# Optimization experiments

Hardware: AMD Instinct MI355X
Metric: run time of the kernel (lower is better)

The kernel has to match this reference:

```python
import jax, jax.numpy as jnp
import numpy as np

N, E, G = 50000, 320000, 256
BN_EPS = 1e-5
HEADS = 4


def _bn(x, g, b):
    # eval-mode BatchNorm1d with running_mean=0, running_var=1
    return g * (x * np.float32(1.0 / np.sqrt(1.0 + BN_EPS))) + b


def _mlp(x, w1, b1, w2, b2):
    return jax.nn.relu(x @ w1 + b1) @ w2 + b2


def _gatv2(x, src, dst, ea, lw, lb, rw, rb, ew, att, bias):
    n = x.shape[0]
    H = HEADS
    C = lw.shape[1] // H
    # self-loops with edge_attr = mean of incoming edge features (fill_value='mean')
    deg = jax.ops.segment_sum(jnp.ones((ea.shape[0],), x.dtype), dst, num_segments=n)
    loop_ea = jax.ops.segment_sum(ea, dst, num_segments=n) / jnp.maximum(deg, 1.0)[:, None]
    ar = jnp.arange(n)
    s = jnp.concatenate([src, ar])
    d = jnp.concatenate([dst, ar])
    ea_all = jnp.concatenate([ea, loop_ea], axis=0)
    xl = (x @ lw + lb).reshape(n, H, C)   # lin_l (source / message features)
    xr = (x @ rw + rb).reshape(n, H, C)   # lin_r (target)
    ee = (ea_all @ ew).reshape(-1, H, C)  # lin_edge (no bias)
    m = jax.nn.leaky_relu(xl[s] + xr[d] + ee, 0.2)       # [E+N, H, C]
    a = jnp.einsum('ehc,hc->eh', m, att)                 # attention logits
    amax = jax.ops.segment_max(a, d, num_segments=n)
    ex = jnp.exp(a - amax[d])
    den = jax.ops.segment_sum(ex, d, num_segments=n)
    w = ex / den[d]                                      # scatter-softmax over target
    out = jax.ops.segment_sum(xl[s] * w[..., None], d, num_segments=n)
    return out.reshape(n, H * C) + bias


def _meta(x, ea, u, src, dst, batch, ep, gp, up):
    # EdgeModel -> NodeModel(GATv2 + relu) -> GlobalModel (residuals=False, eval dropout)
    ea2 = _mlp(jnp.concatenate([x[src], x[dst], ea], axis=1), *ep)
    xn = jax.nn.relu(_gatv2(x, src, dst, ea2, *gp))
    pooled = jax.ops.segment_sum(xn, batch, num_segments=G)
    u2 = _mlp(jnp.concatenate([u, pooled], axis=1), *up)
    return xn, ea2, u2


def _forward(x, edge_attr, e1_w1, e1_b1, e1_w2, e1_b2, g1_lw, g1_lb, g1_rw, g1_rb, g1_ew, g1_att, g1_bias, u1_w1, u1_b1, u1_w2, u1_b2, bn_n_g, bn_n_b, bn_e_g, bn_e_b, bn_u_g, bn_u_b, e2_w1, e2_b1, e2_w2, e2_b2, g2_lw, g2_lb, g2_rw, g2_rb, g2_ew, g2_att, g2_bias, u2_w1, u2_b1, u2_w2, u2_b2, fc1_w, fc1_b, fc2_w, fc2_b, src, dst, batch):
    u0 = jnp.zeros((G, 256), x.dtype)
    x1, ea1, u1 = _meta(x, edge_attr, u0, src, dst, batch,
                        (e1_w1, e1_b1, e1_w2, e1_b2),
                        (g1_lw, g1_lb, g1_rw, g1_rb, g1_ew, g1_att, g1_bias),
                        (u1_w1, u1_b1, u1_w2, u1_b2))
    x1 = _bn(x1, bn_n_g, bn_n_b)
    ea1 = _bn(ea1, bn_e_g, bn_e_b)
    u1 = _bn(u1, bn_u_g, bn_u_b)
    _, _, u2 = _meta(x1, ea1, u1, src, dst, batch,
                     (e2_w1, e2_b1, e2_w2, e2_b2),
                     (g2_lw, g2_lb, g2_rw, g2_rb, g2_ew, g2_att, g2_bias),
                     (u2_w1, u2_b1, u2_w2, u2_b2))
    h = jax.nn.relu(u2 @ fc1_w + fc1_b)
    return h @ fc2_w + fc2_b


def setup_inputs() -> dict:
    key = jax.random.key(0)
    ks = iter(jax.random.split(key, 64))
    rp = lambda shape: jax.random.normal(next(ks), shape, jnp.float32) * 0.05
    inp = {}
    inp['x'] = jax.random.normal(next(ks), (N, 64), jnp.float32)
    inp['edge_attr'] = jax.random.normal(next(ks), (E, 16), jnp.float32)
    # layer 1: EdgeModel(64,16,h=64,out=128), GATv2(64->256,H=4,edge=128), Global(256+256->256)
    inp.update(e1_w1=rp((144, 64)), e1_b1=rp((64,)), e1_w2=rp((64, 128)), e1_b2=rp((128,)))
    inp.update(g1_lw=rp((64, 256)), g1_lb=rp((256,)), g1_rw=rp((64, 256)), g1_rb=rp((256,)),
               g1_ew=rp((128, 256)), g1_att=rp((4, 64)), g1_bias=rp((256,)))
    inp.update(u1_w1=rp((512, 256)), u1_b1=rp((256,)), u1_w2=rp((256, 256)), u1_b2=rp((256,)))
    inp.update(bn_n_g=jnp.ones((256,), jnp.float32), bn_n_b=jnp.zeros((256,), jnp.float32),
               bn_e_g=jnp.ones((128,), jnp.float32), bn_e_b=jnp.zeros((128,), jnp.float32),
               bn_u_g=jnp.ones((256,), jnp.float32), bn_u_b=jnp.zeros((256,), jnp.float32))
    # layer 2: EdgeModel(256,128,h=128,out=128), GATv2(256->256,H=4,edge=128), Global
    inp.update(e2_w1=rp((640, 128)), e2_b1=rp((128,)), e2_w2=rp((128, 128)), e2_b2=rp((128,)))
    inp.update(g2_lw=rp((256, 256)), g2_lb=rp((256,)), g2_rw=rp((256, 256)), g2_rb=rp((256,)),
               g2_ew=rp((128, 256)), g2_att=rp((4, 64)), g2_bias=rp((256,)))
    inp.update(u2_w1=rp((512, 256)), u2_b1=rp((256,)), u2_w2=rp((256, 256)), u2_b2=rp((256,)))
    inp.update(fc1_w=rp((256, 64)), fc1_b=rp((64,)), fc2_w=rp((64, 1)), fc2_b=rp((1,)))
    inp['edge_index'] = jax.random.randint(next(ks), (2, E), 0, N, jnp.int64)
    inp['batch'] = jnp.sort(jax.random.randint(next(ks), (N,), 0, G, jnp.int64))
    return inp


def reference(x, edge_attr, e1_w1, e1_b1, e1_w2, e1_b2, g1_lw, g1_lb, g1_rw, g1_rb, g1_ew, g1_att, g1_bias, u1_w1, u1_b1, u1_w2, u1_b2, bn_n_g, bn_n_b, bn_e_g, bn_e_b, bn_u_g, bn_u_b, e2_w1, e2_b1, e2_w2, e2_b2, g2_lw, g2_lb, g2_rw, g2_rb, g2_ew, g2_att, g2_bias, u2_w1, u2_b1, u2_w2, u2_b2, fc1_w, fc1_b, fc2_w, fc2_b, edge_index, batch):
    return _forward(x, edge_attr, e1_w1, e1_b1, e1_w2, e1_b2, g1_lw, g1_lb, g1_rw, g1_rb, g1_ew, g1_att, g1_bias, u1_w1, u1_b1, u1_w2, u1_b2, bn_n_g, bn_n_b, bn_e_g, bn_e_b, bn_u_g, bn_u_b, e2_w1, e2_b1, e2_w2, e2_b2, g2_lw, g2_lb, g2_rw, g2_rb, g2_ew, g2_att, g2_bias, u2_w1, u2_b1, u2_w2, u2_b2, fc1_w, fc1_b, fc2_w, fc2_b, edge_index[0], edge_index[1], batch)
```

## Files before the change

kernel.cpp:

```cpp
#include <hip/hip_runtime.h>
#include <hip/hip_bf16.h>
#include <hip/hip_fp8.h>
#include <cstdint>
#include <cstddef>

#define INVS 0.99999500003749968f
#define G_GRAPHS 256

using bf16 = __hip_bfloat16;
using short8 = __attribute__((ext_vector_type(8))) short;
using floatx4 = __attribute__((ext_vector_type(4))) float;

__device__ __forceinline__ unsigned short f2bf(float v) {
    union { float f; unsigned u; } x; x.f = v;
    unsigned r = x.u + 0x7fffu + ((x.u >> 16) & 1u);
    return (unsigned short)(r >> 16);
}
__device__ __forceinline__ float bfu(unsigned short u) { return __uint_as_float((unsigned)u << 16); }
__device__ __forceinline__ unsigned char f2fp8(float v) {
    __hip_fp8_e4m3 q(v); return q.__x;
}
__device__ __forceinline__ float fp82f(unsigned char b) {
    __hip_fp8_e4m3 q; q.__x = b; return (float)q;
}

__global__ void degi_k(const int* __restrict__ dst, int* __restrict__ degi, int E) {
    int gid = blockIdx.x * 256 + threadIdx.x;
    if (gid < E) atomicAdd(&degi[dst[gid]], 1);
}

__global__ __launch_bounds__(1024) void scan_blk_k(const int* __restrict__ degi,
                                                   int* __restrict__ off,
                                                   int* __restrict__ bsum, int N) {
    __shared__ int buf[1024];
    int t = threadIdx.x;
    int base = blockIdx.x * 2048;
    int i0 = base + 2 * t, i1 = base + 2 * t + 1;
    int v0 = (i0 < N) ? (degi[i0] + 1) : 0;
    int v1 = (i1 < N) ? (degi[i1] + 1) : 0;
    int s = v0 + v1;
    buf[t] = s;
    __syncthreads();
    for (int ofs = 1; ofs < 1024; ofs <<= 1) {
        int add = (t >= ofs) ? buf[t - ofs] : 0;
        __syncthreads();
        buf[t] += add;
        __syncthreads();
    }
    int excl = buf[t] - s;
    if (i0 < N) off[i0] = excl;
    if (i1 < N) off[i1] = excl + v0;
    if (t == 1023) bsum[blockIdx.x] = buf[1023];
}

__global__ void scan_top_k(const int* __restrict__ bsum, int* __restrict__ boff,
                           int* __restrict__ off, int NBLK, int N) {
    if (threadIdx.x == 0 && blockIdx.x == 0) {
        int run = 0;
        for (int i = 0; i < NBLK; ++i) { boff[i] = run; run += bsum[i]; }
        off[N] = run;
    }
}

__global__ void scan_add_k(int* __restrict__ off, const int* __restrict__ boff, int N) {
    int gid = blockIdx.x * 256 + threadIdx.x;
    if (gid < N) off[gid] += boff[gid >> 11];
}

__global__ void fill_csr_k(const int* __restrict__ src, const int* __restrict__ dst,
                           const int* __restrict__ off, int* __restrict__ fillc,
                           int* __restrict__ csr_src, int* __restrict__ csr_dst,
                           int* __restrict__ csr_eid, int* __restrict__ slot_of,
                           int E, int N) {
    int gid = blockIdx.x * 256 + threadIdx.x;
    if (gid < E) {
        int d = dst[gid];
        int slot = off[d] + atomicAdd(&fillc[d], 1);
        csr_src[slot] = src[gid];
        csr_dst[slot] = d;
        csr_eid[slot] = gid;
        slot_of[gid] = slot;
    }
    if (gid < N) {
        int slot = off[gid + 1] - 1;
        csr_src[slot] = gid;
        csr_dst[slot] = gid;
        csr_eid[slot] = E + gid;
    }
}

__global__ void conv_weights1_k(const float* __restrict__ w1, const float* __restrict__ w2,
                                short* __restrict__ w1s, short* __restrict__ w2s) {
    int gid = blockIdx.x * 256 + threadIdx.x;
    if (gid < 1280) {
        int f = gid >> 6, lane = gid & 63;
        int kk = f >> 2, tt = f & 3;
        int n = tt * 16 + (lane & 15);
        int k0 = kk * 32 + (lane >> 4) * 8;
        short8 v;
        for (int j = 0; j < 8; ++j) {
            int k = k0 + j;
            v[j] = (k < 144) ? (short)f2bf(w1[k * 64 + n]) : (short)0;
        }
        *(short8*)(w1s + (long long)gid * 8) = v;
    } else if (gid < 2304) {
        int g2 = gid - 1280;
        int f = g2 >> 6, lane = g2 & 63;
        int kk = f >> 3, tt = f & 7;
        int n = tt * 16 + (lane & 15);
        int k0 = kk * 32 + (lane >> 4) * 8;
        short8 v;
        for (int j = 0; j < 8; ++j) v[j] = (short)f2bf(w2[(k0 + j) * 128 + n]);
        *(short8*)(w2s + (long long)g2 * 8) = v;
    }
}

__global__ void conv_ew_k(const float* __restrict__ ew, short* __restrict__ ews) {
    int gid = blockIdx.x * 256 + threadIdx.x;
    if (gid >= 4096) return;
    int f = gid >> 6, lane = gid & 63;
    int kk = f >> 4, tt = f & 15;
    int n = tt * 16 + (lane & 15);
    int k0 = kk * 32 + (lane >> 4) * 8;
    short8 v;
    for (int j = 0; j < 8; ++j) v[j] = (short)f2bf(ew[(k0 + j) * 256 + n]);
    *(short8*)(ews + (long long)gid * 8) = v;
}

template <int K>
__global__ void conv_nodew_k(const float* __restrict__ wl, const float* __restrict__ wr,
                             short* __restrict__ out) {
    int gid = blockIdx.x * 256 + threadIdx.x;
    if (gid >= (K / 32) * 32 * 64) return;
    int f = gid >> 6, lane = gid & 63;
    int kk = f >> 5, tt = f & 31;
    int n = tt * 16 + (lane & 15);
    int k0 = kk * 32 + (lane >> 4) * 8;
    short8 v;
    for (int j = 0; j < 8; ++j) {
        int k = k0 + j;
        float x = (n < 256) ? wl[k * 256 + n] : wr[k * 256 + (n - 256)];
        v[j] = (short)f2bf(x);
    }
    *(short8*)(out + (long long)gid * 8) = v;
}

__global__ void conv_pre2w_k(const float* __restrict__ w1, short* __restrict__ out) {
    int gid = blockIdx.x * 256 + threadIdx.x;
    if (gid >= 8 * 16 * 64) return;
    int f = gid >> 6, lane = gid & 63;
    int kk = f >> 4, tt = f & 15;
    int n = tt * 16 + (lane & 15);
    int k0 = kk * 32 + (lane >> 4) * 8;
    short8 v;
    for (int j = 0; j < 8; ++j) {
        int k = k0 + j;
        float x = (n < 128) ? w1[k * 128 + n] : w1[(256 + k) * 128 + (n - 128)];
        v[j] = (short)f2bf(x);
    }
    *(short8*)(out + (long long)gid * 8) = v;
}

__global__ __launch_bounds__(256) void edge_mlp1_mfma_k(
    const float* __restrict__ x, const float* __restrict__ ea,
    const int* __restrict__ src, const int* __restrict__ dst,
    const int* __restrict__ slot_of,
    const short* __restrict__ w1s, const float* __restrict__ b1,
    const short* __restrict__ w2s, const float* __restrict__ b2,
    const short* __restrict__ ews,
    bf16* __restrict__ out, unsigned char* __restrict__ ee8, int E) {
    __shared__ short At[32][168];
    __shared__ short Ht[32][72];
    __shared__ unsigned char Et[32][272];
    __shared__ int sdv[32][2];
    __shared__ int slt[32];
    int t = threadIdx.x;
    long long e0 = (long long)blockIdx.x * 32;
    if (t < 64) {
        int r = t & 31;
        long long e = e0 + r;
        int v = 0;
        if (e < E) v = (t < 32) ? src[e] : dst[e];
        sdv[r][t >> 5] = v;
    } else if (t < 96) {
        int r = t - 64;
        long long e = e0 + r;
        slt[r] = (e < E) ? slot_of[e] : -1;
    }
    __syncthreads();
    for (int i = t; i < 32 * 40; i += 256) {
        int r = i / 40, c = i - r * 40;
        long long e = e0 + r;
        float4 v = {0.f, 0.f, 0.f, 0.f};
        if (e < E) {
            if (c < 16)      v = *(const float4*)(x + (long long)sdv[r][0] * 64 + c * 4);
            else if (c < 32) v = *(const float4*)(x + (long long)sdv[r][1] * 64 + (c - 16) * 4);
            else if (c < 36) v = *(const float4*)(ea + e * 16 + (c - 32) * 4);
        }
        ushort4 pk;
        pk.x = f2bf(v.x); pk.y = f2bf(v.y); pk.z = f2bf(v.z); pk.w = f2bf(v.w);
        *(ushort4*)&At[r][c * 4] = pk;
    }
    __syncthreads();

    int w = t >> 6, lane = t & 63;
    int m0 = (w & 1) * 16;
    int lr = lane & 15, lq = lane >> 4;

    int nq1 = (w >> 1) * 2;
    floatx4 acc[2];
    for (int i = 0; i < 2; ++i) acc[i] = (floatx4){0.f, 0.f, 0.f, 0.f};
    for (int kk = 0; kk < 5; ++kk) {
        short8 a = *(const short8*)&At[m0 + lr][kk * 32 + lq * 8];
        for (int tt = 0; tt < 2; ++tt) {
            short8 b = *(const short8*)(w1s + ((long long)((kk * 4 + nq1 + tt) * 64 + lane)) * 8);
            acc[tt] = __builtin_amdgcn_mfma_f32_16x16x32_bf16(a, b, acc[tt], 0, 0, 0);
        }
    }
    for (int tt = 0; tt < 2; ++tt) {
        int col = (nq1 + tt) * 16 + lr;
        float bv = b1[col];
        for (int r = 0; r < 4; ++r)
            Ht[m0 + lq * 4 + r][col] = (short)f2bf(fmaxf(acc[tt][r] + bv, 0.f));
    }
    __syncthreads();

    int nq2 = (w >> 1) * 4;
    floatx4 acc2[4];
    for (int i = 0; i < 4; ++i) acc2[i] = (floatx4){0.f, 0.f, 0.f, 0.f};
    for (int kk = 0; kk < 2; ++kk) {
        short8 a = *(const short8*)&Ht[m0 + lr][kk * 32 + lq * 8];
        for (int tt = 0; tt < 4; ++tt) {
            short8 b = *(const short8*)(w2s + ((long long)((kk * 8 + nq2 + tt) * 64 + lane)) * 8);
            acc2[tt] = __builtin_amdgcn_mfma_f32_16x16x32_bf16(a, b, acc2[tt], 0, 0, 0);
        }
    }
    for (int tt = 0; tt < 4; ++tt) {
        int col = (nq2 + tt) * 16 + lr;
        float bv = b2[col];
        for (int r = 0; r < 4; ++r)
            At[m0 + lq * 4 + r][col] = (short)f2bf(acc2[tt][r] + bv);
    }
    __syncthreads();
    {
        int nq3 = (w >> 1) * 8;
        floatx4 acc3[8];
        for (int i = 0; i < 8; ++i) acc3[i] = (floatx4){0.f, 0.f, 0.f, 0.f};
        for (int kk = 0; kk < 4; ++kk) {
            short8 a = *(const short8*)&At[m0 + lr][kk * 32 + lq * 8];
            for (int tt = 0; tt < 8; ++tt) {
                short8 b = *(const short8*)(ews + ((long long)((kk * 16 + nq3 + tt) * 64 + lane)) * 8);
                acc3[tt] = __builtin_amdgcn_mfma_f32_16x16x32_bf16(a, b, acc3[tt], 0, 0, 0);
            }
        }
        for (int tt = 0; tt < 8; ++tt) {
            int col = (nq3 + tt) * 16 + lr;
            for (int r = 0; r < 4; ++r)
                Et[m0 + lq * 4 + r][col] = f2fp8(acc3[tt][r]);
        }
    }
    for (int i = t; i < 512; i += 256) {
        int r = i >> 4, c = i & 15;
        int s = slt[r];
        if (s >= 0)
            *(short8*)(void*)(out + (long long)s * 128 + c * 8) = *(const short8*)&At[r][c * 8];
    }
    __syncthreads();
    for (int i = t; i < 512; i += 256) {
        int r = i >> 4, c = i & 15;
        int s = slt[r];
        if (s >= 0)
            *(uint4*)(ee8 + (long long)s * 256 + c * 16) = *(const uint4*)&Et[r][c * 16];
    }
}

template <int K, typename T>
__global__ __launch_bounds__(256) void node_linear_mfma_k(
    const T* x, const short* __restrict__ ws,
    const float* __restrict__ bl, const float* __restrict__ br,
    bf16* __restrict__ xl, bf16* xr, int N) {
    __shared__ short At[16][K + 8];
    __shared__ short Ot[16][520];
    int t = threadIdx.x;
    long long n0 = (long long)blockIdx.x * 16;
    if (sizeof(T) == 4) {
        for (int i = t; i < 16 * (K / 4); i += 256) {
            int r = i / (K / 4), c = i % (K / 4);
            long long n = n0 + r;
            float4 v = {0.f, 0.f, 0.f, 0.f};
            if (n < N) v = *(const float4*)((const float*)x + n * K + c * 4);
            ushort4 pk;
            pk.x = f2bf(v.x); pk.y = f2bf(v.y); pk.z = f2bf(v.z); pk.w = f2bf(v.w);
            *(ushort4*)&At[r][c * 4] = pk;
        }
    } else {
        for (int i = t; i < 16 * (K / 8); i += 256) {
            int r = i / (K / 8), c = i % (K / 8);
            long long n = n0 + r;
            short8 v = {0, 0, 0, 0, 0, 0, 0, 0};
            if (n < N) v = *(const short8*)(const void*)((const bf16*)x + n * K + c * 8);
            *(short8*)&At[r][c * 8] = v;
        }
    }
    __syncthreads();

    int w = t >> 6, lane = t & 63;
    int nq = w * 8;
    int lr = lane & 15, lq = lane >> 4;

    floatx4 acc[8];
    for (int i = 0; i < 8; ++i) acc[i] = (floatx4){0.f, 0.f, 0.f, 0.f};
    for (int kk = 0; kk < K / 32; ++kk) {
        short8 a = *(const short8*)&At[lr][kk * 32 + lq * 8];
        for (int tt = 0; tt < 8; ++tt) {
            short8 b = *(const short8*)(ws + ((long long)((kk * 32 + nq + tt) * 64 + lane)) * 8);
            acc[tt] = __builtin_amdgcn_mfma_f32_16x16x32_bf16(a, b, acc[tt], 0, 0, 0);
        }
    }
    for (int tt = 0; tt < 8; ++tt) {
        int col = (nq + tt) * 16 + lr;
        float bv = (col < 256) ? bl[col] : br[col - 256];
        for (int r = 0; r < 4; ++r)
            Ot[lq * 4 + r][col] = (short)f2bf(acc[tt][r] + bv);
    }
    __syncthreads();
    for (int i = t; i < 1024; i += 256) {
        int r = i >> 6, c = i & 63;
        long long n = n0 + r;
        if (n < N) {
            short8 v = *(const short8*)&Ot[r][c * 8];
            if (c < 32) *(short8*)(void*)(xl + n * 256 + c * 8) = v;
            else        *(short8*)(void*)(xr + n * 256 + (c - 32) * 8) = v;
        }
    }
}

__global__ __launch_bounds__(256) void pre_mfma_k(
    const bf16* __restrict__ x, const short* __restrict__ ws,
    const float* __restrict__ bx, bf16* __restrict__ out, int N) {
    __shared__ short At[16][264];
    __shared__ short Ot[16][264];
    int t = threadIdx.x;
    long long n0 = (long long)blockIdx.x * 16;
    for (int i = t; i < 512; i += 256) {
        int r = i >> 5, c = i & 31;
        long long n = n0 + r;
        short8 v = {0, 0, 0, 0, 0, 0, 0, 0};
        if (n < N) v = *(const short8*)(const void*)(x + n * 256 + c * 8);
        *(short8*)&At[r][c * 8] = v;
    }
    __syncthreads();

    int w = t >> 6, lane = t & 63;
    int nq = w * 4;
    int lr = lane & 15, lq = lane >> 4;

    floatx4 acc[4];
    for (int i = 0; i < 4; ++i) acc[i] = (floatx4){0.f, 0.f, 0.f, 0.f};
    for (int kk = 0; kk < 8; ++kk) {
        short8 a = *(const short8*)&At[lr][kk * 32 + lq * 8];
        for (int tt = 0; tt < 4; ++tt) {
            short8 b = *(const short8*)(ws + ((long long)((kk * 16 + nq + tt) * 64 + lane)) * 8);
            acc[tt] = __builtin_amdgcn_mfma_f32_16x16x32_bf16(a, b, acc[tt], 0, 0, 0);
        }
    }
    for (int tt = 0; tt < 4; ++tt) {
        int col = (nq + tt) * 16 + lr;
        float bv = bx[col];
        for (int r = 0; r < 4; ++r)
            Ot[lq * 4 + r][col] = (short)f2bf(acc[tt][r] + bv);
    }
    __syncthreads();
    for (int i = t; i < 512; i += 256) {
        int r = i >> 5, c = i & 31;
        long long n = n0 + r;
        if (n < N)
            *(short8*)(void*)(out + n * 256 + c * 8) = *(const short8*)&Ot[r][c * 8];
    }
}

template <bool L1>
__global__ __launch_bounds__(256) void gat_fused_k(
    const unsigned char* __restrict__ ee8, const bf16* __restrict__ xl, const bf16* xr,
    const int* __restrict__ off, const int* __restrict__ csr_src,
    const float* __restrict__ att, const float* __restrict__ bias,
    const float* __restrict__ bng, const float* __restrict__ bnb,
    const int* __restrict__ batch,
    bf16* x1bn, float* __restrict__ pooled, int N) {
    __shared__ float ps[4][260];
    __shared__ int bid[4];
    int t = threadIdx.x;
    int w = t >> 6, lane = t & 63;
    int n = blockIdx.x * 4 + w;
    bool valid = n < N;
    int c0 = lane * 4;
    float o0 = 0.f, o1 = 0.f, o2 = 0.f, o3 = 0.f;
    if (valid) {
        ushort4 xrp = *(const ushort4*)(const void*)(xr + (long long)n * 256 + c0);
        ushort4 xop = *(const ushort4*)(const void*)(xl + (long long)n * 256 + c0);
        float xr0 = bfu(xrp.x), xr1 = bfu(xrp.y), xr2 = bfu(xrp.z), xr3 = bfu(xrp.w);
        float4 atv = *(const float4*)(att + c0);
        float a0 = 0.f, a1 = 0.f, a2 = 0.f, a3 = 0.f, dacc = 0.f;
        float es0 = 0.f, es1 = 0.f, es2 = 0.f, es3 = 0.f;
        int beg = off[n], end1 = off[n + 1] - 1;
        ushort4 xlp;
        unsigned ep;
        {
            int sid = csr_src[beg];
            xlp = *(const ushort4*)(const void*)(xl + (long long)sid * 256 + c0);
            ep = *(const unsigned*)(ee8 + (long long)beg * 256 + c0);
        }
        for (int i = beg; i < end1; ++i) {
            ushort4 cx = xlp;
            unsigned ce = ep;
            if (i + 1 < end1) {
                int sid = csr_src[i + 1];
                xlp = *(const ushort4*)(const void*)(xl + (long long)sid * 256 + c0);
                ep = *(const unsigned*)(ee8 + (long long)(i + 1) * 256 + c0);
            }
            float x0 = bfu(cx.x), x1 = bfu(cx.y), x2 = bfu(cx.z), x3 = bfu(cx.w);
            float e0 = fp82f(ce & 0xff);
            float e1 = fp82f((ce >> 8) & 0xff);
            float e2 = fp82f((ce >> 16) & 0xff);
            float e3 = fp82f(ce >> 24);
            es0 += e0; es1 += e1; es2 += e2; es3 += e3;
            float m0 = x0 + xr0 + e0;
            float m1 = x1 + xr1 + e1;
            float m2 = x2 + xr2 + e2;
            float m3 = x3 + xr3 + e3;
            m0 = m0 > 0.f ? m0 : 0.2f * m0;
            m1 = m1 > 0.f ? m1 : 0.2f * m1;
            m2 = m2 > 0.f ? m2 : 0.2f * m2;
            m3 = m3 > 0.f ? m3 : 0.2f * m3;
            float p = atv.x * m0 + atv.y * m1 + atv.z * m2 + atv.w * m3;
            p += __shfl_xor(p, 1, 64);
            p += __shfl_xor(p, 2, 64);
            p += __shfl_xor(p, 4, 64);
            p += __shfl_xor(p, 8, 64);
            float ex = expf(p);
            a0 += ex * x0; a1 += ex * x1; a2 += ex * x2; a3 += ex * x3;
            dacc += ex;
        }
        {
            float rdv = 1.f / fmaxf((float)(end1 - beg), 1.f);
            float x0 = bfu(xop.x), x1 = bfu(xop.y), x2 = bfu(xop.z), x3 = bfu(xop.w);
            float m0 = x0 + xr0 + es0 * rdv;
            float m1 = x1 + xr1 + es1 * rdv;
            float m2 = x2 + xr2 + es2 * rdv;
            float m3 = x3 + xr3 + es3 * rdv;
            m0 = m0 > 0.f ? m0 : 0.2f * m0;
            m1 = m1 > 0.f ? m1 : 0.2f * m1;
            m2 = m2 > 0.f ? m2 : 0.2f * m2;
            m3 = m3 > 0.f ? m3 : 0.2f * m3;
            float p = atv.x * m0 + atv.y * m1 + atv.z * m2 + atv.w * m3;
            p += __shfl_xor(p, 1, 64);
            p += __shfl_xor(p, 2, 64);
            p += __shfl_xor(p, 4, 64);
            p += __shfl_xor(p, 8, 64);
            float ex = expf(p);
            a0 += ex * x0; a1 += ex * x1; a2 += ex * x2; a3 += ex * x3;
            dacc += ex;
        }
        float inv = 1.f / dacc;
        o0 = fmaxf(a0 * inv + bias[c0],     0.f);
        o1 = fmaxf(a1 * inv + bias[c0 + 1], 0.f);
        o2 = fmaxf(a2 * inv + bias[c0 + 2], 0.f);
        o3 = fmaxf(a3 * inv + bias[c0 + 3], 0.f);
        if (L1) {
            ushort4 o;
            o.x = f2bf(bng[c0]     * (o0 * INVS) + bnb[c0]);
            o.y = f2bf(bng[c0 + 1] * (o1 * INVS) + bnb[c0 + 1]);
            o.z = f2bf(bng[c0 + 2] * (o2 * INVS) + bnb[c0 + 2]);
            o.w = f2bf(bng[c0 + 3] * (o3 * INVS) + bnb[c0 + 3]);
            *(ushort4*)(void*)(x1bn + (long long)n * 256 + c0) = o;
        }
    }
    if (lane == 0) bid[w] = valid ? batch[n] : -1;
    ps[w][c0]     = o0;
    ps[w][c0 + 1] = o1;
    ps[w][c0 + 2] = o2;
    ps[w][c0 + 3] = o3;
    __syncthreads();
    int b0 = bid[0];
    bool same = (b0 >= 0)
             && (bid[1] < 0 || bid[1] == b0)
             && (bid[2] < 0 || bid[2] == b0)
             && (bid[3] < 0 || bid[3] == b0);
    if (same) {
        float s = ps[0][t] + ps[1][t] + ps[2][t] + ps[3][t];
        atomicAdd(&pooled[(long long)b0 * 256 + t], s);
    } else if (valid) {
        long long pb = (long long)bid[w] * 256 + c0;
        atomicAdd(&pooled[pb],     o0);
        atomicAdd(&pooled[pb + 1], o1);
        atomicAdd(&pooled[pb + 2], o2);
        atomicAdd(&pooled[pb + 3], o3);
    }
}

__global__ void global_mlp1_k(const float* __restrict__ pooled,
                              const float* __restrict__ w1, const float* __restrict__ b1,
                              const float* __restrict__ w2, const float* __restrict__ b2,
                              const float* __restrict__ bng, const float* __restrict__ bnb,
                              float* __restrict__ u1bn) {
    __shared__ float pr[256];
    __shared__ float h[256];
    int t = threadIdx.x, g = blockIdx.x;
    pr[t] = pooled[g * 256 + t];
    __syncthreads();
    float acc = b1[t];
    for (int k = 0; k < 256; ++k) acc += pr[k] * w1[(256 + k) * 256 + t];
    h[t] = fmaxf(acc, 0.f);
    __syncthreads();
    float a2 = b2[t];
    for (int k = 0; k < 256; ++k) a2 += h[k] * w2[k * 256 + t];
    u1bn[g * 256 + t] = bng[t] * (a2 * INVS) + bnb[t];
}

__global__ void conv_weights_k(const float* __restrict__ w1, const float* __restrict__ w2,
                               const float* __restrict__ b1,
                               const float* __restrict__ bg, const float* __restrict__ bb,
                               short* __restrict__ w1s, short* __restrict__ w2s,
                               float* __restrict__ b1x) {
    int gid = blockIdx.x * 256 + threadIdx.x;
    if (gid < 10240) {
        int f = gid >> 6, lane = gid & 63;
        int kk = f >> 3, tt = f & 7;
        int n = tt * 16 + (lane & 15);
        int k0 = kk * 32 + (lane >> 4) * 8;
        short8 v;
        for (int j = 0; j < 8; ++j) {
            int k = k0 + j;
            float x = w1[k * 128 + n];
            if (k >= 512) x *= bg[k - 512] * INVS;
            v[j] = (short)f2bf(x);
        }
        *(short8*)(w1s + (long long)gid * 8) = v;
    } else if (gid < 12288) {
        int g2 = gid - 10240;
        int f = g2 >> 6, lane = g2 & 63;
        int kk = f >> 3, tt = f & 7;
        int n = tt * 16 + (lane & 15);
        int k0 = kk * 32 + (lane >> 4) * 8;
        short8 v;
        for (int j = 0; j < 8; ++j) v[j] = (short)f2bf(w2[(k0 + j) * 128 + n]);
        *(short8*)(w2s + (long long)g2 * 8) = v;
    } else if (gid < 12544) {
        int j = gid - 12288;
        b1x[j] = 0.f;
    } else if (gid < 12672) {
        int j = gid - 12544;
        float acc = b1[j];
        for (int c = 0; c < 128; ++c) acc += bb[c] * w1[(512 + c) * 128 + j];
        b1x[128 + j] = acc;
    }
}

__global__ __launch_bounds__(256) void edge_mlp2_mfma_k(
    const bf16* __restrict__ xpre, const bf16* __restrict__ ea_slot,
    const int* __restrict__ csr_src, const int* __restrict__ csr_dst,
    const int* __restrict__ csr_eid,
    const short* __restrict__ w1s,
    const short* __restrict__ w2s, const float* __restrict__ b2,
    const short* __restrict__ ews,
    unsigned char* __restrict__ ee8, int NT, int E) {
    __shared__ float Ps[32][132];
    __shared__ short At[32][136];
    __shared__ short Ht[32][136];
    __shared__ int sdv[32][3];
    unsigned char* Et = (unsigned char*)&Ps[0][0];
    int t = threadIdx.x;
    long long s0 = (long long)blockIdx.x * 32;
    if (t < 96) {
        int r = t & 31, which = t >> 5;
        long long s = s0 + r;
        int v = (which == 2) ? E : 0;
        if (s < NT) v = (which == 0) ? csr_src[s] : (which == 1 ? csr_dst[s] : csr_eid[s]);
        sdv[r][which] = v;
    }
    __syncthreads();
    for (int i = t; i < 512; i += 256) {
        int r = i >> 4, c = i & 15;
        long long s = s0 + r;
        bool ok = (s < NT) && (sdv[r][2] < E);
        float p[8];
        if (ok) {
            short8 vs = *(const short8*)(const void*)(xpre + (long long)sdv[r][0] * 256 + c * 8);
            short8 vd = *(const short8*)(const void*)(xpre + (long long)sdv[r][1] * 256 + 128 + c * 8);
            for (int j = 0; j < 8; ++j)
                p[j] = bfu((unsigned short)vs[j]) + bfu((unsigned short)vd[j]);
        } else {
            for (int j = 0; j < 8; ++j) p[j] = 0.f;
        }
        for (int j = 0; j < 8; ++j) Ps[r][c * 8 + j] = p[j];
    }
    for (int i = t; i < 512; i += 256) {
        int r = i >> 4, c = i & 15;
        long long s = s0 + r;
        short8 v = {0, 0, 0, 0, 0, 0, 0, 0};
        if (s < NT && sdv[r][2] < E)
            v = *(const short8*)(const void*)(ea_slot + s * 128 + c * 8);
        *(short8*)&At[r][c * 8] = v;
    }
    __syncthreads();

    int w = t >> 6, lane = t & 63;
    int m0 = (w & 1) * 16;
    int nq = (w >> 1) * 4;
    int lr = lane & 15, lq = lane >> 4;

    floatx4 acc[4];
    for (int tt = 0; tt < 4; ++tt) {
        int col = (nq + tt) * 16 + lr;
        for (int r = 0; r < 4; ++r) acc[tt][r] = Ps[m0 + lq * 4 + r][col];
    }
    for (int kk = 0; kk < 4; ++kk) {
        short8 a = *(const short8*)&At[m0 + lr][kk * 32 + lq * 8];
        for (int tt = 0; tt < 4; ++tt) {
            short8 b = *(const short8*)(w1s + ((long long)(((16 + kk) * 8 + nq + tt) * 64 + lane)) * 8);
            acc[tt] = __builtin_amdgcn_mfma_f32_16x16x32_bf16(a, b, acc[tt], 0, 0, 0);
        }
    }
    for (int tt = 0; tt < 4; ++tt) {
        int col = (nq + tt) * 16 + lr;
        for (int r = 0; r < 4; ++r)
            Ht[m0 + lq * 4 + r][col] = (short)f2bf(fmaxf(acc[tt][r], 0.f));
    }
    __syncthreads();

    floatx4 acc2[4];
    for (int i = 0; i < 4; ++i) acc2[i] = (floatx4){0.f, 0.f, 0.f, 0.f};
    for (int kk = 0; kk < 4; ++kk) {
        short8 a = *(const short8*)&Ht[m0 + lr][kk * 32 + lq * 8];
        for (int tt = 0; tt < 4; ++tt) {
            short8 b = *(const short8*)(w2s + ((long long)((kk * 8 + nq + tt) * 64 + lane)) * 8);
            acc2[tt] = __builtin_amdgcn_mfma_f32_16x16x32_bf16(a, b, acc2[tt], 0, 0, 0);
        }
    }
    for (int tt = 0; tt < 4; ++tt) {
        int col = (nq + tt) * 16 + lr;
        float bv = b2[col];
        for (int r = 0; r < 4; ++r)
            At[m0 + lq * 4 + r][col] = (short)f2bf(acc2[tt][r] + bv);
    }
    __syncthreads();
    {
        int nq3 = (w >> 1) * 8;
        floatx4 acc3[8];
        for (int i = 0; i < 8; ++i) acc3[i] = (floatx4){0.f, 0.f, 0.f, 0.f};
        for (int kk = 0; kk < 4; ++kk) {
            short8 a = *(const short8*)&At[m0 + lr][kk * 32 + lq * 8];
            for (int tt = 0; tt < 8; ++tt) {
                short8 b = *(const short8*)(ews + ((long long)((kk * 16 + nq3 + tt) * 64 + lane)) * 8);
                acc3[tt] = __builtin_amdgcn_mfma_f32_16x16x32_bf16(a, b, acc3[tt], 0, 0, 0);
            }
        }
        for (int tt = 0; tt < 8; ++tt) {
            int col = (nq3 + tt) * 16 + lr;
            for (int r = 0; r < 4; ++r)
                Et[(m0 + lq * 4 + r) * 272 + col] = f2fp8(acc3[tt][r]);
        }
    }
    __syncthreads();
    for (int i = t; i < 512; i += 256) {
        int r = i >> 4, c = i & 15;
        long long s = s0 + r;
        if (s < NT && sdv[r][2] < E)
            *(uint4*)(ee8 + s * 256 + c * 16) = *(const uint4*)(Et + r * 272 + c * 16);
    }
}

__global__ void final_mlp_k(const float* __restrict__ u1bn, const float* __restrict__ pooled,
                            const float* __restrict__ w1, const float* __restrict__ b1,
                            const float* __restrict__ w2, const float* __restrict__ b2,
                            const float* __restrict__ f1w, const float* __restrict__ f1b,
                            const float* __restrict__ f2w, const float* __restrict__ f2b,
                            float* __restrict__ out) {
    __shared__ float ub[256], pb[256], h[256], u2[256];
    int t = threadIdx.x, g = blockIdx.x;
    ub[t] = u1bn[g * 256 + t];
    pb[t] = pooled[g * 256 + t];
    __syncthreads();
    float acc = b1[t];
    for (int k = 0; k < 256; ++k)
        acc += ub[k] * w1[k * 256 + t] + pb[k] * w1[(256 + k) * 256 + t];
    h[t] = fmaxf(acc, 0.f);
    __syncthreads();
    float a2 = b2[t];
    for (int k = 0; k < 256; ++k) a2 += h[k] * w2[k * 256 + t];
    u2[t] = a2;
    __syncthreads();
    float fv = 0.f;
    if (t < 64) {
        float a3 = f1b[t];
        for (int k = 0; k < 256; ++k) a3 += u2[k] * f1w[k * 64 + t];
        fv = fmaxf(a3, 0.f) * f2w[t];
    }
    for (int off = 32; off; off >>= 1) fv += __shfl_down(fv, off, 64);
    if (t == 0) out[g] = fv + f2b[0];
}

extern "C" void kernel_launch(void* const* d_in, const int* in_sizes, int n_in,
                              void* d_out, int out_size, void* d_ws, size_t ws_size,
                              hipStream_t stream) {
    const float* x         = (const float*)d_in[0];
    const float* edge_attr = (const float*)d_in[1];
    const float* e1_w1 = (const float*)d_in[2];
    const float* e1_b1 = (const float*)d_in[3];
    const float* e1_w2 = (const float*)d_in[4];
    const float* e1_b2 = (const float*)d_in[5];
    const float* g1_lw = (const float*)d_in[6];
    const float* g1_lb = (const float*)d_in[7];
    const float* g1_rw = (const float*)d_in[8];
    const float* g1_rb = (const float*)d_in[9];
    const float* g1_ew = (const float*)d_in[10];
    const float* g1_att = (const float*)d_in[11];
    const float* g1_bias = (const float*)d_in[12];
    const float* u1_w1 = (const float*)d_in[13];
    const float* u1_b1 = (const float*)d_in[14];
    const float* u1_w2 = (const float*)d_in[15];
    const float* u1_b2 = (const float*)d_in[16];
    const float* bn_n_g = (const float*)d_in[17];
    const float* bn_n_b = (const float*)d_in[18];
    const float* bn_e_g = (const float*)d_in[19];
    const float* bn_e_b = (const float*)d_in[20];
    const float* bn_u_g = (const float*)d_in[21];
    const float* bn_u_b = (const float*)d_in[22];
    const float* e2_w1 = (const float*)d_in[23];
    const float* e2_b1 = (const float*)d_in[24];
    const float* e2_w2 = (const float*)d_in[25];
    const float* e2_b2 = (const float*)d_in[26];
    const float* g2_lw = (const float*)d_in[27];
    const float* g2_lb = (const float*)d_in[28];
    const float* g2_rw = (const float*)d_in[29];
    const float* g2_rb = (const float*)d_in[30];
    const float* g2_ew = (const float*)d_in[31];
    const float* g2_att = (const float*)d_in[32];
    const float* g2_bias = (const float*)d_in[33];
    const float* u2_w1 = (const float*)d_in[34];
    const float* u2_b1 = (const float*)d_in[35];
    const float* u2_w2 = (const float*)d_in[36];
    const float* u2_b2 = (const float*)d_in[37];
    const float* fc1_w = (const float*)d_in[38];
    const float* fc1_b = (const float*)d_in[39];
    const float* fc2_w = (const float*)d_in[40];
    const float* fc2_b = (const float*)d_in[41];
    const int* edge_index = (const int*)d_in[42];
    const int* batch = (const int*)d_in[43];

    const int N = in_sizes[0] / 64;
    const int E = in_sizes[1] / 16;
    const int NT = E + N;
    const int G = G_GRAPHS;
    const int* src = edge_index;
    const int* dst = edge_index + E;
    const int NB = (NT + 31) / 32;
    const int NSB = (N + 2047) / 2048;

    char* p = (char*)d_ws;
    auto alloc = [&](size_t bytes) { char* r = p; p += (bytes + 255) & ~(size_t)255; return r; };
    bf16* eabuf = (bf16*)alloc((size_t)NT * 128 * 2);
    bf16* xl    = (bf16*)alloc((size_t)N * 256 * 2);
    bf16* xr    = (bf16*)alloc((size_t)N * 256 * 2);
    bf16* x1bn  = xr;
    unsigned char* ee8 = (unsigned char*)alloc((size_t)NT * 256);
    int* degi   = (int*)alloc((size_t)N * 4);
    int* off    = (int*)alloc((size_t)(N + 1) * 4);
    int* fillc  = (int*)alloc((size_t)N * 4);
    int* csr_src = (int*)alloc((size_t)NT * 4);
    int* csr_dst = (int*)alloc((size_t)NT * 4);
    int* csr_eid = (int*)alloc((size_t)NT * 4);
    int* slot_of = (int*)alloc((size_t)E * 4);
    int* bsum   = (int*)alloc((size_t)(NSB + 1) * 4);
    int* boff   = (int*)alloc((size_t)(NSB + 1) * 4);
    float* pooled = (float*)alloc((size_t)G * 256 * 4);
    float* u1bn = (float*)alloc((size_t)G * 256 * 4);
    short* w1s  = (short*)alloc((size_t)20 * 8 * 64 * 8 * 2);
    short* w2s  = (short*)alloc((size_t)4 * 8 * 64 * 8 * 2);
    float* b1x  = (float*)alloc((size_t)256 * 4);
    short* w1s1 = (short*)alloc((size_t)5 * 4 * 64 * 8 * 2);
    short* w2s1 = (short*)alloc((size_t)2 * 8 * 64 * 8 * 2);
    short* ews1 = (short*)alloc((size_t)4 * 16 * 64 * 8 * 2);
    short* ews2 = (short*)alloc((size_t)4 * 16 * 64 * 8 * 2);
    short* nw1  = (short*)alloc((size_t)2 * 32 * 64 * 8 * 2);
    short* nw2  = (short*)alloc((size_t)8 * 32 * 64 * 8 * 2);
    short* nwp  = (short*)alloc((size_t)8 * 16 * 64 * 8 * 2);

    hipMemsetAsync(degi, 0, (size_t)N * 4, stream);
    hipMemsetAsync(fillc, 0, (size_t)N * 4, stream);
    hipMemsetAsync(pooled, 0, (size_t)G * 256 * 4, stream);
    degi_k<<<(E + 255) / 256, 256, 0, stream>>>(dst, degi, E);
    scan_blk_k<<<NSB, 1024, 0, stream>>>(degi, off, bsum, N);
    scan_top_k<<<1, 64, 0, stream>>>(bsum, boff, off, NSB, N);
    scan_add_k<<<(N + 255) / 256, 256, 0, stream>>>(off, boff, N);
    fill_csr_k<<<(max(E, N) + 255) / 256, 256, 0, stream>>>(src, dst, off, fillc,
                                                            csr_src, csr_dst, csr_eid,
                                                            slot_of, E, N);

    conv_weights1_k<<<9, 256, 0, stream>>>(e1_w1, e1_w2, w1s1, w2s1);
    conv_ew_k<<<16, 256, 0, stream>>>(g1_ew, ews1);
    conv_ew_k<<<16, 256, 0, stream>>>(g2_ew, ews2);
    conv_nodew_k<64><<<16, 256, 0, stream>>>(g1_lw, g1_rw, nw1);
    conv_nodew_k<256><<<64, 256, 0, stream>>>(g2_lw, g2_rw, nw2);
    conv_pre2w_k<<<32, 256, 0, stream>>>(e2_w1, nwp);
    edge_mlp1_mfma_k<<<(E + 31) / 32, 256, 0, stream>>>(x, edge_attr, src, dst, slot_of,
                                                        w1s1, e1_b1, w2s1, e1_b2, ews1,
                                                        eabuf, ee8, E);
    node_linear_mfma_k<64, float><<<(N + 15) / 16, 256, 0, stream>>>(x, nw1, g1_lb, g1_rb, xl, xr, N);
    gat_fused_k<true><<<(N + 3) / 4, 256, 0, stream>>>(ee8, xl, xr, off, csr_src,
                                                       g1_att, g1_bias, bn_n_g, bn_n_b,
                                                       batch, x1bn, pooled, N);
    global_mlp1_k<<<G, 256, 0, stream>>>(pooled, u1_w1, u1_b1, u1_w2, u1_b2, bn_u_g, bn_u_b, u1bn);

    conv_weights_k<<<50, 256, 0, stream>>>(e2_w1, e2_w2, e2_b1, bn_e_g, bn_e_b, w1s, w2s, b1x);
    pre_mfma_k<<<(N + 15) / 16, 256, 0, stream>>>(x1bn, nwp, b1x, xl, N);
    edge_mlp2_mfma_k<<<NB, 256, 0, stream>>>(xl, eabuf, csr_src, csr_dst, csr_eid,
                                             w1s, w2s, e2_b2, ews2, ee8, NT, E);
    node_linear_mfma_k<256, bf16><<<(N + 15) / 16, 256, 0, stream>>>(x1bn, nw2, g2_lb, g2_rb, xl, xr, N);
    hipMemsetAsync(pooled, 0, (size_t)G * 256 * 4, stream);
    gat_fused_k<false><<<(N + 3) / 4, 256, 0, stream>>>(ee8, xl, xr, off, csr_src,
                                                        g2_att, g2_bias, nullptr, nullptr,
                                                        batch, nullptr, pooled, N);
    final_mlp_k<<<G, 256, 0, stream>>>(u1bn, pooled, u2_w1, u2_b1, u2_w2, u2_b2,
                                       fc1_w, fc1_b, fc2_w, fc2_b, (float*)d_out);
}
```

Measured before the change: 847.5 us.

## Precompute per-node first-layer edge MLP projections and iterate edges in CSR order

The first edge MLP layer is split algebraically. x[src]@W1a and x[dst]@W1b + b1 are now computed once per node in a new pre1 kernel, so each edge only gathers two bf16 128-wide rows, adds them, and runs a small K=16 MFMA for the edge-attribute part. The edge kernel now walks CSR slots directly rather than scattering through slot_of, so its stores are contiguous. Self-loop slots are processed with zero inputs. This adds an extra kernel and N×128 bf16 buffer and rounds the node projections to bf16 before summing.

```diff
diff --git a/kernel.cpp b/kernel.cpp
--- a/kernel.cpp
+++ b/kernel.cpp
@@ -70,8 +70,7 @@
 __global__ void fill_csr_k(const int* __restrict__ src, const int* __restrict__ dst,
                            const int* __restrict__ off, int* __restrict__ fillc,
                            int* __restrict__ csr_src, int* __restrict__ csr_dst,
-                           int* __restrict__ csr_eid, int* __restrict__ slot_of,
-                           int E, int N) {
+                           int* __restrict__ csr_eid, int E, int N) {
     int gid = blockIdx.x * 256 + threadIdx.x;
     if (gid < E) {
         int d = dst[gid];
@@ -79,7 +78,6 @@
         csr_src[slot] = src[gid];
         csr_dst[slot] = d;
         csr_eid[slot] = gid;
-        slot_of[gid] = slot;
     }
     if (gid < N) {
         int slot = off[gid + 1] - 1;
@@ -90,19 +88,32 @@
 }
 
 __global__ void conv_weights1_k(const float* __restrict__ w1, const float* __restrict__ w2,
-                                short* __restrict__ w1s, short* __restrict__ w2s) {
+                                short* __restrict__ w1p, short* __restrict__ w1c,
+                                short* __restrict__ w2s) {
     int gid = blockIdx.x * 256 + threadIdx.x;
-    if (gid < 1280) {
+    if (gid < 1024) {
         int f = gid >> 6, lane = gid & 63;
-        int kk = f >> 2, tt = f & 3;
+        int kk = f >> 3, tt = f & 7;
         int n = tt * 16 + (lane & 15);
         int k0 = kk * 32 + (lane >> 4) * 8;
         short8 v;
         for (int j = 0; j < 8; ++j) {
             int k = k0 + j;
-            v[j] = (k < 144) ? (short)f2bf(w1[k * 64 + n]) : (short)0;
-        }
-        *(short8*)(w1s + (long long)gid * 8) = v;
+            float x = (n < 64) ? w1[k * 64 + n] : w1[(64 + k) * 64 + (n - 64)];
+            v[j] = (short)f2bf(x);
+        }
+        *(short8*)(w1p + (long long)gid * 8) = v;
+    } else if (gid < 1280) {
+        int g2 = gid - 1024;
+        int tt = g2 >> 6, lane = g2 & 63;
+        int n = tt * 16 + (lane & 15);
+        int k0 = (lane >> 4) * 8;
+        short8 v;
+        for (int j = 0; j < 8; ++j) {
+            int k = k0 + j;
+            v[j] = (k < 16) ? (short)f2bf(w1[(128 + k) * 64 + n]) : (short)0;
+        }
+        *(short8*)(w1c + (long long)g2 * 8) = v;
     } else if (gid < 2304) {
         int g2 = gid - 1280;
         int f = g2 >> 6, lane = g2 & 63;
@@ -161,93 +172,155 @@
     *(short8*)(out + (long long)gid * 8) = v;
 }
 
-__global__ __launch_bounds__(256) void edge_mlp1_mfma_k(
-    const float* __restrict__ x, const float* __restrict__ ea,
-    const int* __restrict__ src, const int* __restrict__ dst,
-    const int* __restrict__ slot_of,
-    const short* __restrict__ w1s, const float* __restrict__ b1,
-    const short* __restrict__ w2s, const float* __restrict__ b2,
-    const short* __restrict__ ews,
-    bf16* __restrict__ out, unsigned char* __restrict__ ee8, int E) {
-    __shared__ short At[32][168];
-    __shared__ short Ht[32][72];
-    __shared__ unsigned char Et[32][272];
-    __shared__ int sdv[32][2];
-    __shared__ int slt[32];
+__global__ __launch_bounds__(256) void pre1_mfma_k(
+    const float* __restrict__ x, const short* __restrict__ w1p,
+    const float* __restrict__ b1, bf16* __restrict__ pre1, int N) {
+    __shared__ short At[16][72];
+    __shared__ short Ot[16][136];
     int t = threadIdx.x;
-    long long e0 = (long long)blockIdx.x * 32;
-    if (t < 64) {
-        int r = t & 31;
-        long long e = e0 + r;
-        int v = 0;
-        if (e < E) v = (t < 32) ? src[e] : dst[e];
-        sdv[r][t >> 5] = v;
-    } else if (t < 96) {
-        int r = t - 64;
-        long long e = e0 + r;
-        slt[r] = (e < E) ? slot_of[e] : -1;
-    }
-    __syncthreads();
-    for (int i = t; i < 32 * 40; i += 256) {
-        int r = i / 40, c = i - r * 40;
-        long long e = e0 + r;
+    long long n0 = (long long)blockIdx.x * 16;
+    {
+        int r = t >> 4, c = t & 15;
+        long long n = n0 + r;
         float4 v = {0.f, 0.f, 0.f, 0.f};
-        if (e < E) {
-            if (c < 16)      v = *(const float4*)(x + (long long)sdv[r][0] * 64 + c * 4);
-            else if (c < 32) v = *(const float4*)(x + (long long)sdv[r][1] * 64 + (c - 16) * 4);
-            else if (c < 36) v = *(const float4*)(ea + e * 16 + (c - 32) * 4);
-        }
+        if (n < N) v = *(const float4*)(x + n * 64 + c * 4);
         ushort4 pk;
         pk.x = f2bf(v.x); pk.y = f2bf(v.y); pk.z = f2bf(v.z); pk.w = f2bf(v.w);
         *(ushort4*)&At[r][c * 4] = pk;
     }
     __syncthreads();
+    int w = t >> 6, lane = t & 63;
+    int nq = w * 2;
+    int lr = lane & 15, lq = lane >> 4;
+    floatx4 acc[2];
+    for (int i = 0; i < 2; ++i) acc[i] = (floatx4){0.f, 0.f, 0.f, 0.f};
+    for (int kk = 0; kk < 2; ++kk) {
+        short8 a = *(const short8*)&At[lr][kk * 32 + lq * 8];
+        for (int tt = 0; tt < 2; ++tt) {
+            short8 b = *(const short8*)(w1p + ((long long)((kk * 8 + nq + tt) * 64 + lane)) * 8);
+            acc[tt] = __builtin_amdgcn_mfma_f32_16x16x32_bf16(a, b, acc[tt], 0, 0, 0);
+        }
+    }
+    for (int tt = 0; tt < 2; ++tt) {
+        int col = (nq + tt) * 16 + lr;
+        float bv = (col >= 64) ? b1[col - 64] : 0.f;
+        for (int r = 0; r < 4; ++r)
+            Ot[lq * 4 + r][col] = (short)f2bf(acc[tt][r] + bv);
+    }
+    __syncthreads();
+    {
+        int r = t >> 4, c = t & 15;
+        long long n = n0 + r;
+        if (n < N)
+            *(short8*)(void*)(pre1 + n * 128 + c * 8) = *(const short8*)&Ot[r][c * 8];
+    }
+}
+
+__global__ __launch_bounds__(256) void edge_mlp1_mfma_k(
+    const bf16* __restrict__ pre1, const float* __restrict__ ea,
+    const int* __restrict__ csr_src, const int* __restrict__ csr_dst,
+    const int* __restrict__ csr_eid,
+    const short* __restrict__ w1c,
+    const short* __restrict__ w2s, const float* __restrict__ b2,
+    const short* __restrict__ ews,
+    bf16* __restrict__ out, unsigned char* __restrict__ ee8, int NT, int E) {
+    __shared__ float Ps[32][68];
+    __shared__ short Ae[32][40];
+    __shared__ short Ht[32][72];
+    __shared__ short A2[32][136];
+    __shared__ int sdv[32][3];
+    unsigned char* Et = (unsigned char*)&Ps[0][0];
+    int t = threadIdx.x;
+    long long s0 = (long long)blockIdx.x * 32;
+    if (t < 96) {
+        int r = t & 31, which = t >> 5;
+        long long s = s0 + r;
+        int v = (which == 2) ? E : 0;
+        if (s < NT) v = (which == 0) ? csr_src[s] : (which == 1 ? csr_dst[s] : csr_eid[s]);
+        sdv[r][which] = v;
+    }
+    __syncthreads();
+    {
+        int r = t >> 3, c = t & 7;
+        long long s = s0 + r;
+        bool ok = (s < NT) && (sdv[r][2] < E);
+        float p[8];
+        if (ok) {
+            short8 vs = *(const short8*)(const void*)(pre1 + (long long)sdv[r][0] * 128 + c * 8);
+            short8 vd = *(const short8*)(const void*)(pre1 + (long long)sdv[r][1] * 128 + 64 + c * 8);
+            for (int j = 0; j < 8; ++j)
+                p[j] = bfu((unsigned short)vs[j]) + bfu((unsigned short)vd[j]);
+        } else {
+            for (int j = 0; j < 8; ++j) p[j] = 0.f;
+        }
+        for (int j = 0; j < 8; ++j) Ps[r][c * 8 + j] = p[j];
+    }
+    if (t < 128) {
+        int r = t >> 2, c = t & 3;
+        long long s = s0 + r;
+        int eid = sdv[r][2];
+        float4 v = {0.f, 0.f, 0.f, 0.f};
+        if (s < NT && eid < E) v = *(const float4*)(ea + (long long)eid * 16 + c * 4);
+        ushort4 pk;
+        pk.x = f2bf(v.x); pk.y = f2bf(v.y); pk.z = f2bf(v.z); pk.w = f2bf(v.w);
+        *(ushort4*)&Ae[r][c * 4] = pk;
+    } else {
+        int i = t - 128;
+        int r = i >> 2, c = i & 3;
+        *(ushort4*)&Ae[r][16 + c * 4] = (ushort4){0, 0, 0, 0};
+    }
+    __syncthreads();
 
     int w = t >> 6, lane = t & 63;
     int m0 = (w & 1) * 16;
     int lr = lane & 15, lq = lane >> 4;
 
-    int nq1 = (w >> 1) * 2;
-    floatx4 acc[2];
-    for (int i = 0; i < 2; ++i) acc[i] = (floatx4){0.f, 0.f, 0.f, 0.f};
-    for (int kk = 0; kk < 5; ++kk) {
-        short8 a = *(const short8*)&At[m0 + lr][kk * 32 + lq * 8];
+    {
+        int nq1 = (w >> 1) * 2;
+        floatx4 acc[2];
         for (int tt = 0; tt < 2; ++tt) {
-            short8 b = *(const short8*)(w1s + ((long long)((kk * 4 + nq1 + tt) * 64 + lane)) * 8);
+            int col = (nq1 + tt) * 16 + lr;
+            for (int r = 0; r < 4; ++r) acc[tt][r] = Ps[m0 + lq * 4 + r][col];
+        }
+        short8 a = *(const short8*)&Ae[m0 + lr][lq * 8];
+        for (int tt = 0; tt < 2; ++tt) {
+            short8 b = *(const short8*)(w1c + ((long long)((nq1 + tt) * 64 + lane)) * 8);
             acc[tt] = __builtin_amdgcn_mfma_f32_16x16x32_bf16(a, b, acc[tt], 0, 0, 0);
         }
-    }
-    for (int tt = 0; tt < 2; ++tt) {
-        int col = (nq1 + tt) * 16 + lr;
-        float bv = b1[col];
-        for (int r = 0; r < 4; ++r)
-            Ht[m0 + lq * 4 + r][col] = (short)f2bf(fmaxf(acc[tt][r] + bv, 0.f));
-    }
-    __syncthreads();
-
-    int nq2 = (w >> 1) * 4;
-    floatx4 acc2[4];
-    for (int i = 0; i < 4; ++i) acc2[i] = (floatx4){0.f, 0.f, 0.f, 0.f};
-    for (int kk = 0; kk < 2; ++kk) {
-        short8 a = *(const short8*)&Ht[m0 + lr][kk * 32 + lq * 8];
+        for (int tt = 0; tt < 2; ++tt) {
+            int col = (nq1 + tt) * 16 + lr;
+            for (int r = 0; r < 4; ++r)
+                Ht[m0 + lq * 4 + r][col] = (short)f2bf(fmaxf(acc[tt][r], 0.f));
+        }
+    }
+    __syncthreads();
+
+    {
+        int nq2 = (w >> 1) * 4;
+        floatx4 acc2[4];
+        for (int i = 0; i < 4; ++i) acc2[i] = (floatx4){0.f, 0.f, 0.f, 0.f};
+        for (int kk = 0; kk < 2; ++kk) {
+            short8 a = *(const short8*)&Ht[m0 + lr][kk * 32 + lq * 8];
+            for (int tt = 0; tt < 4; ++tt) {
+                short8 b = *(const short8*)(w2s + ((long long)((kk * 8 + nq2 + tt) * 64 + lane)) * 8);
+                acc2[tt] = __builtin_amdgcn_mfma_f32_16x16x32_bf16(a, b, acc2[tt], 0, 0, 0);
+            }
+        }
         for (int tt = 0; tt < 4; ++tt) {
-            short8 b = *(const short8*)(w2s + ((long long)((kk * 8 + nq2 + tt) * 64 + lane)) * 8);
-            acc2[tt] = __builtin_amdgcn_mfma_f32_16x16x32_bf16(a, b, acc2[tt], 0, 0, 0);
-        }
-    }
-    for (int tt = 0; tt < 4; ++tt) {
-        int col = (nq2 + tt) * 16 + lr;
-        float bv = b2[col];
-        for (int r = 0; r < 4; ++r)
-            At[m0 + lq * 4 + r][col] = (short)f2bf(acc2[tt][r] + bv);
-    }
-    __syncthreads();
+            int col = (nq2 + tt) * 16 + lr;
+            float bv = b2[col];
+            for (int r = 0; r < 4; ++r)
+                A2[m0 + lq * 4 + r][col] = (short)f2bf(acc2[tt][r] + bv);
+        }
+    }
+    __syncthreads();
+
     {
         int nq3 = (w >> 1) * 8;
         floatx4 acc3[8];
         for (int i = 0; i < 8; ++i) acc3[i] = (floatx4){0.f, 0.f, 0.f, 0.f};
         for (int kk = 0; kk < 4; ++kk) {
-            short8 a = *(const short8*)&At[m0 + lr][kk * 32 + lq * 8];
+            short8 a = *(const short8*)&A2[m0 + lr][kk * 32 + lq * 8];
             for (int tt = 0; tt < 8; ++tt) {
                 short8 b = *(const short8*)(ews + ((long long)((kk * 16 + nq3 + tt) * 64 + lane)) * 8);
                 acc3[tt] = __builtin_amdgcn_mfma_f32_16x16x32_bf16(a, b, acc3[tt], 0, 0, 0);
@@ -256,21 +329,21 @@
         for (int tt = 0; tt < 8; ++tt) {
             int col = (nq3 + tt) * 16 + lr;
             for (int r = 0; r < 4; ++r)
-                Et[m0 + lq * 4 + r][col] = f2fp8(acc3[tt][r]);
+                Et[(m0 + lq * 4 + r) * 272 + col] = f2fp8(acc3[tt][r]);
         }
     }
     for (int i = t; i < 512; i += 256) {
         int r = i >> 4, c = i & 15;
-        int s = slt[r];
-        if (s >= 0)
-            *(short8*)(void*)(out + (long long)s * 128 + c * 8) = *(const short8*)&At[r][c * 8];
+        long long s = s0 + r;
+        if (s < NT)
+            *(short8*)(void*)(out + s * 128 + c * 8) = *(const short8*)&A2[r][c * 8];
     }
     __syncthreads();
     for (int i = t; i < 512; i += 256) {
         int r = i >> 4, c = i & 15;
-        int s = slt[r];
-        if (s >= 0)
-            *(uint4*)(ee8 + (long long)s * 256 + c * 16) = *(const uint4*)&Et[r][c * 16];
+        long long s = s0 + r;
+        if (s < NT)
+            *(uint4*)(ee8 + s * 256 + c * 16) = *(const uint4*)(Et + r * 272 + c * 16);
     }
 }
 
@@ -764,13 +837,13 @@
     bf16* xr    = (bf16*)alloc((size_t)N * 256 * 2);
     bf16* x1bn  = xr;
     unsigned char* ee8 = (unsigned char*)alloc((size_t)NT * 256);
+    bf16* pre1  = (bf16*)alloc((size_t)N * 128 * 2);
     int* degi   = (int*)alloc((size_t)N * 4);
     int* off    = (int*)alloc((size_t)(N + 1) * 4);
     int* fillc  = (int*)alloc((size_t)N * 4);
     int* csr_src = (int*)alloc((size_t)NT * 4);
     int* csr_dst = (int*)alloc((size_t)NT * 4);
     int* csr_eid = (int*)alloc((size_t)NT * 4);
-    int* slot_of = (int*)alloc((size_t)E * 4);
     int* bsum   = (int*)alloc((size_t)(NSB + 1) * 4);
     int* boff   = (int*)alloc((size_t)(NSB + 1) * 4);
     float* pooled = (float*)alloc((size_t)G * 256 * 4);
@@ -778,8 +851,9 @@
     short* w1s  = (short*)alloc((size_t)20 * 8 * 64 * 8 * 2);
     short* w2s  = (short*)alloc((size_t)4 * 8 * 64 * 8 * 2);
     float* b1x  = (float*)alloc((size_t)256 * 4);
-    short* w1s1 = (short*)alloc((size_t)5 * 4 * 64 * 8 * 2);
-    short* w2s1 = (short*)alloc((size_t)2 * 8 * 64 * 8 * 2);
+    short* w1p  = (short*)alloc((size_t)16 * 64 * 8 * 2);
+    short* w1c  = (short*)alloc((size_t)4 * 64 * 8 * 2);
+    short* w2s1 = (short*)alloc((size_t)16 * 64 * 8 * 2);
     short* ews1 = (short*)alloc((size_t)4 * 16 * 64 * 8 * 2);
     short* ews2 = (short*)alloc((size_t)4 * 16 * 64 * 8 * 2);
     short* nw1  = (short*)alloc((size_t)2 * 32 * 64 * 8 * 2);
@@ -794,18 +868,17 @@
     scan_top_k<<<1, 64, 0, stream>>>(bsum, boff, off, NSB, N);
     scan_add_k<<<(N + 255) / 256, 256, 0, stream>>>(off, boff, N);
     fill_csr_k<<<(max(E, N) + 255) / 256, 256, 0, stream>>>(src, dst, off, fillc,
-                                                            csr_src, csr_dst, csr_eid,
-                                                            slot_of, E, N);
-
-    conv_weights1_k<<<9, 256, 0, stream>>>(e1_w1, e1_w2, w1s1, w2s1);
+                                                            csr_src, csr_dst, csr_eid, E, N);
+
+    conv_weights1_k<<<9, 256, 0, stream>>>(e1_w1, e1_w2, w1p, w1c, w2s1);
     conv_ew_k<<<16, 256, 0, stream>>>(g1_ew, ews1);
     conv_ew_k<<<16, 256, 0, stream>>>(g2_ew, ews2);
     conv_nodew_k<64><<<16, 256, 0, stream>>>(g1_lw, g1_rw, nw1);
     conv_nodew_k<256><<<64, 256, 0, stream>>>(g2_lw, g2_rw, nw2);
     conv_pre2w_k<<<32, 256, 0, stream>>>(e2_w1, nwp);
-    edge_mlp1_mfma_k<<<(E + 31) / 32, 256, 0, stream>>>(x, edge_attr, src, dst, slot_of,
-                                                        w1s1, e1_b1, w2s1, e1_b2, ews1,
-                                                        eabuf, ee8, E);
+    pre1_mfma_k<<<(N + 15) / 16, 256, 0, stream>>>(x, w1p, e1_b1, pre1, N);
+    edge_mlp1_mfma_k<<<NB, 256, 0, stream>>>(pre1, edge_attr, csr_src, csr_dst, csr_eid,
+                                             w1c, w2s1, e1_b2, ews1, eabuf, ee8, NT, E);
     node_linear_mfma_k<64, float><<<(N + 15) / 16, 256, 0, stream>>>(x, nw1, g1_lb, g1_rb, xl, xr, N);
     gat_fused_k<true><<<(N + 3) / 4, 256, 0, stream>>>(ee8, xl, xr, off, csr_src,
                                                        g1_att, g1_bias, bn_n_g, bn_n_b,
```

Measured after the change: 826.5 us. 1.03x faster.
